# Performance work log

Measured on AMD Instinct MI355X. Metric: run time of the kernel, lower is better.

## Reference

```python
import jax, jax.numpy as jnp
import numpy as np

B, N, D, FF, L = 32, 1000, 128, 512, 6
EPS = 1e-5  # InstanceNorm1d default eps


def _inorm(x, g, b):
    # InstanceNorm1d on [B, d, N] == normalize over sequence dim N per channel (biased var)
    m = jnp.mean(x, axis=1, keepdims=True)
    v = jnp.var(x, axis=1, keepdims=True)
    return (x - m) / jnp.sqrt(v + EPS) * g + b


def setup_inputs() -> dict:
    key = jax.random.key(0)
    ks = jax.random.split(key, 10)
    s = 0.05
    data = jax.random.normal(ks[0], (B, N, 2), dtype=jnp.float32)
    # negative pairwise distances (module calls it negative_dist)
    dist = -jax.random.uniform(ks[1], (B, N, N), dtype=jnp.float32)
    log_scale = jnp.ones((1,), dtype=jnp.float32)
    We = jax.random.normal(ks[2], (D, 2), dtype=jnp.float32) * s
    be = jnp.zeros((D,), dtype=jnp.float32)
    Wq = jax.random.normal(ks[3], (L, D, D), dtype=jnp.float32) * s
    Wk = jax.random.normal(ks[4], (L, D, D), dtype=jnp.float32) * s
    Wv = jax.random.normal(ks[5], (L, D, D), dtype=jnp.float32) * s
    g1 = jnp.ones((L, D), dtype=jnp.float32)
    b1 = jnp.zeros((L, D), dtype=jnp.float32)
    W1 = jax.random.normal(ks[6], (L, FF, D), dtype=jnp.float32) * s
    bw1 = jnp.zeros((L, FF), dtype=jnp.float32)
    W2 = jax.random.normal(ks[7], (L, D, FF), dtype=jnp.float32) * s
    bw2 = jnp.zeros((L, D), dtype=jnp.float32)
    g2 = jnp.ones((L, D), dtype=jnp.float32)
    b2 = jnp.zeros((L, D), dtype=jnp.float32)
    alpha = jnp.ones((L,), dtype=jnp.float32)  # AFT_dist_alpha per layer
    return dict(data=data, dist=dist, log_scale=log_scale, We=We, be=be,
                Wq=Wq, Wk=Wk, Wv=Wv, g1=g1, b1=b1, W1=W1, bw1=bw1,
                W2=W2, bw2=bw2, g2=g2, b2=b2, alpha=alpha)


def reference(data, dist, log_scale, We, be, Wq, Wk, Wv, g1, b1, W1, bw1, W2, bw2, g2, b2, alpha):
    x = data @ We.T + be  # [B,N,D]
    for i in range(L):
        q = x @ Wq[i].T
        k = x @ Wk[i].T
        v = x @ Wv[i].T
        A = jnp.exp(log_scale[0] * alpha[i] * dist)  # [B,N,N]
        ek = jnp.exp(k)
        bias = jnp.einsum('bnm,bmd->bnd', A, ek * v)
        denom = jnp.einsum('bnm,bmd->bnd', A, ek)
        out = jax.nn.sigmoid(q) * (bias / denom)
        x1 = _inorm(x + out, g1[i], b1[i])
        h = jax.nn.relu(x1 @ W1[i].T + bw1[i]) @ W2[i].T + bw2[i]
        x = _inorm(x1 + h, g2[i], b2[i])
    return x
```

## Files before the change

kernel.cpp:

```cpp
#include <hip/hip_runtime.h>
#include <hip/hip_bf16.h>

typedef __attribute__((ext_vector_type(4))) float f32x4;
typedef __attribute__((ext_vector_type(8))) short bf16x8;
typedef __attribute__((ext_vector_type(4))) short s16x4;

#define LCOUNT 6

static __device__ __forceinline__ unsigned short f2b(float f){
  __hip_bfloat16 h = __float2bfloat16(f);
  return __builtin_bit_cast(unsigned short, h);
}
static __device__ __forceinline__ float b2f(unsigned short u){
  unsigned int x = ((unsigned int)u) << 16;
  return __builtin_bit_cast(float, x);
}
static __device__ __forceinline__ void gl16(const void* g, void* l){
  __builtin_amdgcn_global_load_lds(
      (const __attribute__((address_space(1))) void*)g,
      (__attribute__((address_space(3))) void*)l, 16, 0, 0);
}
static __device__ __forceinline__ f32x4 mfma16(bf16x8 a, bf16x8 b, f32x4 c){
  return __builtin_amdgcn_mfma_f32_16x16x32_bf16(a, b, c, 0, 0, 0);
}

__global__ void k_cvt5(const float* __restrict__ Wq, const float* __restrict__ Wk,
                       const float* __restrict__ Wv, const float* __restrict__ W1,
                       const float* __restrict__ W2,
                       unsigned short* __restrict__ wqb, unsigned short* __restrict__ wkb,
                       unsigned short* __restrict__ wvb, unsigned short* __restrict__ w1b,
                       unsigned short* __restrict__ w2b){
  int i = blockIdx.x*256 + threadIdx.x;
  if (i < 98304) wqb[i] = f2b(Wq[i]);
  else if (i < 196608) wkb[i-98304] = f2b(Wk[i-98304]);
  else if (i < 294912) wvb[i-196608] = f2b(Wv[i-196608]);
  else if (i < 688128) w1b[i-294912] = f2b(W1[i-294912]);
  else w2b[i-688128] = f2b(W2[i-688128]);
}

__global__ void k_cvtdist(const float* __restrict__ dist, unsigned short* __restrict__ db){
  int t = blockIdx.x*256 + threadIdx.x;
  int row = t >> 7, ch = t & 127;
  bf16x8 w;
  if (ch >= 125){
#pragma unroll
    for (int e=0;e<8;e++) w[e] = 0;
  } else {
    const float* p = dist + (size_t)row*1000 + ch*8;
    f32x4 a = *(const f32x4*)p;
    f32x4 b = *(const f32x4*)(p + 4);
#pragma unroll
    for (int e=0;e<4;e++){ w[e] = (short)f2b(a[e]); w[4+e] = (short)f2b(b[e]); }
  }
  *(bf16x8*)&db[(size_t)row*1024 + ch*8] = w;
}

__global__ void k_embed(const float* __restrict__ data, const float* __restrict__ We,
                        const float* __restrict__ be, float* __restrict__ x,
                        unsigned short* __restrict__ xb){
  int idx = blockIdx.x*256 + threadIdx.x;
  int d = idx & 127, bn = idx >> 7;
  float v = data[bn*2]*We[d*2] + data[bn*2+1]*We[d*2+1] + be[d];
  x[idx] = v; xb[idx] = f2b(v);
}

__global__ void k_scale(const float* __restrict__ part, int cnt,
                        const float* __restrict__ g, const float* __restrict__ beta,
                        float* __restrict__ na, float* __restrict__ nc){
  int b = blockIdx.x, d = threadIdx.x;
  float s1 = 0.f, s2 = 0.f;
  for (int c = 0; c < cnt; ++c){
    size_t pi = (((size_t)b*cnt + c)*128 + d)*2;
    s1 += part[pi]; s2 += part[pi+1];
  }
  float mean = s1 * 1e-3f;
  float var  = s2 * 1e-3f - mean*mean;
  float a = g[d] * rsqrtf(var + 1e-5f);
  na[b*128 + d] = a; nc[b*128 + d] = beta[d] - mean*a;
}

__global__ __launch_bounds__(256) void k_fapply(
  const float* __restrict__ x, const float* __restrict__ na,
  const float* __restrict__ nc, float* __restrict__ dout){
  int blk = blockIdx.x, tid = threadIdx.x;
  int b = blk / 125;
  size_t base = (size_t)blk*1024 + tid*4;
  int d0 = (tid*4) & 127;
  f32x4 v = *(const f32x4*)&x[base];
  f32x4 o;
#pragma unroll
  for (int e=0;e<4;e++) o[e] = v[e]*na[b*128 + d0 + e] + nc[b*128 + d0 + e];
  *(f32x4*)&dout[base] = o;
}

template<int NORM>
__global__ __launch_bounds__(256) void k_qkv(
  const unsigned short* __restrict__ xb, const float* __restrict__ x,
  const float* __restrict__ na2, const float* __restrict__ nc2,
  const unsigned short* __restrict__ Wqb, const unsigned short* __restrict__ Wkb,
  const unsigned short* __restrict__ Wvb,
  unsigned short* __restrict__ sigq, unsigned short* __restrict__ Zc)
{
  __shared__ unsigned short LA[2*2048];
  __shared__ unsigned short LB[2][4][256][8];
  __shared__ float sna[128], snc[128];
  int tid = threadIdx.x, wid = tid>>6, lane = tid&63;
  int l15 = lane&15, lg = lane>>4;
  int wm = wid>>1, wn = wid&1;
  int bt = blockIdx.x, b = bt>>4, t = bt&15;
  int kv = blockIdx.y;
  int lrow = t*64 + lane; if (lrow > 999) lrow = 999;
  size_t arow = (size_t)(b*1000 + lrow);

  if (NORM){
    if (tid < 128){ sna[tid] = na2[b*128 + tid]; snc[tid] = nc2[b*128 + tid]; }
    __syncthreads();
  }

  f32x4 zf = {0.f,0.f,0.f,0.f};
  f32x4 acc[2][4], acc2[2][4];
#pragma unroll
  for (int i=0;i<2;i++)
#pragma unroll
    for (int j=0;j<4;j++){ acc[i][j] = zf; acc2[i][j] = zf; }

  auto stage = [&](int kk, int buf){
    int k0 = kk*32;
    if (NORM){
      const float* p = x + arow*128 + k0 + wid*8;
      f32x4 v0 = *(const f32x4*)p;
      f32x4 v1 = *(const f32x4*)(p + 4);
      bf16x8 w;
#pragma unroll
      for (int e=0;e<4;e++){
        int k = k0 + wid*8;
        w[e]   = (short)f2b(v0[e]*sna[k+e]   + snc[k+e]);
        w[4+e] = (short)f2b(v1[e]*sna[k+4+e] + snc[k+4+e]);
      }
      *(bf16x8*)&LA[buf*2048 + wid*512 + lane*8] = w;
    } else {
      gl16(xb + arow*128 + k0 + wid*8, &LA[buf*2048 + wid*512]);
    }
    if (kv == 0){
#pragma unroll
      for (int t2=0;t2<2;++t2){
        int e = wid + t2*4, g2 = e>>1, nb = e&1;
        gl16(Wqb + (size_t)(nb*64+lane)*128 + k0 + g2*8, &LB[buf][g2][nb*64][0]);
      }
    } else {
#pragma unroll
      for (int t2=0;t2<4;++t2){
        int e = wid + t2*4, g2 = e&3, nb = e>>2;
        const unsigned short* src = (nb < 2)
          ? Wkb + (size_t)(nb*64+lane)*128 + k0 + g2*8
          : Wvb + (size_t)((nb-2)*64+lane)*128 + k0 + g2*8;
        gl16(src, &LB[buf][g2][nb*64][0]);
      }
    }
  };
  auto compute = [&](int buf){
    bf16x8 af[2];
#pragma unroll
    for (int i=0;i<2;i++){
      int row = wm*32 + i*16 + l15;
      af[i] = *(const bf16x8*)&LA[buf*2048 + lg*512 + row*8];
    }
#pragma unroll
    for (int j=0;j<4;j++){
      bf16x8 bq = *(const bf16x8*)&LB[buf][lg][wn*64 + j*16 + l15][0];
#pragma unroll
      for (int i=0;i<2;i++) acc[i][j] = mfma16(af[i], bq, acc[i][j]);
      if (kv){
        bf16x8 bv = *(const bf16x8*)&LB[buf][lg][128 + wn*64 + j*16 + l15][0];
#pragma unroll
        for (int i=0;i<2;i++) acc2[i][j] = mfma16(af[i], bv, acc2[i][j]);
      }
    }
  };

  stage(0, 0);
  __syncthreads();
  for (int kk = 0; kk < 4; ++kk){
    int buf = kk & 1;
    if (kk < 3) stage(kk+1, buf^1);
    compute(buf);
    __syncthreads();
  }

#pragma unroll
  for (int i=0;i<2;i++){
    int m4 = t*64 + wm*32 + i*16 + lg*4;
    if (m4 >= 1000) continue;
#pragma unroll
    for (int j=0;j<4;j++){
      int col = wn*64 + j*16 + l15;
      if (kv == 0){
#pragma unroll
        for (int r=0;r<4;r++)
          sigq[(size_t)(b*1000 + m4 + r)*128 + col] = f2b(1.f/(1.f + __expf(-acc[i][j][r])));
      } else {
        s16x4 pv, pk;
#pragma unroll
        for (int r=0;r<4;r++){
          float ek = __expf(acc[i][j][r]);
          pk[r] = (short)f2b(ek);
          pv[r] = (short)f2b(ek * acc2[i][j][r]);
        }
        size_t base = ((size_t)(b*128 + (m4>>3))*256 + col)*8 + ((m4>>2)&1)*4;
        *(s16x4*)&Zc[base] = pv;
        *(s16x4*)&Zc[base + 1024] = pk;
      }
    }
  }
}

template<int NORM, int USE16>
__global__ __launch_bounds__(256) void k_attn(
  const float* __restrict__ dist, const unsigned short* __restrict__ db16,
  const unsigned short* __restrict__ Zc, const unsigned short* __restrict__ sigq,
  float* __restrict__ x, float* __restrict__ partA,
  const float* __restrict__ na2, const float* __restrict__ nc2,
  const float* __restrict__ log_scale, const float* __restrict__ alpha, int layer)
{
  union SM {
    struct { unsigned short A[2][8][64][8]; unsigned short B[2][8][256][8]; } st;
    float den[64][128];
  };
  __shared__ SM sm;
  int tid = threadIdx.x, wid = tid>>6, lane = tid&63;
  int l15 = lane&15, lg = lane>>4;
  int bb = blockIdx.y, t = blockIdx.x, n0 = t*64;
  float sc = log_scale[0]*alpha[layer];
  const unsigned short* Zb = Zc + ((size_t)bb << 18);
  int an = n0 + lane; if (an > 999) an = 999;
  const size_t drow = (size_t)(bb*1000 + an);

  f32x4 zf = {0.f,0.f,0.f,0.f};
  f32x4 acc[4][4];
#pragma unroll
  for (int i=0;i<4;i++)
#pragma unroll
    for (int j=0;j<4;j++) acc[i][j] = zf;

  auto issueB = [&](int kk, int buf){
#pragma unroll
    for (int t2=0;t2<8;++t2){
      int e = wid + t2*4;
      int g2 = e >> 2, cb = e & 3;
      gl16(Zb + ((size_t)((kk*8 + g2)*256 + cb*64 + lane))*8, &sm.st.B[buf][g2][cb*64][0]);
    }
  };
  auto loadA2 = [&](int kk, float* v0, float* v1){
    int k0 = kk*64 + wid*8;
    int k1 = k0 + 32;
    if (USE16){
      bf16x8 r0 = *(const bf16x8*)(db16 + drow*1024 + k0);
      bf16x8 r1 = *(const bf16x8*)(db16 + drow*1024 + k1);
#pragma unroll
      for (int e=0;e<8;e++){ v0[e] = b2f((unsigned short)r0[e]); v1[e] = b2f((unsigned short)r1[e]); }
    } else {
      const float* dp = dist + drow*1000;
#pragma unroll
      for (int e=0;e<8;e++){
        int m0 = k0 + e; if (m0 > 999) m0 = 999;
        int m1 = k1 + e; if (m1 > 999) m1 = 999;
        v0[e] = dp[m0]; v1[e] = dp[m1];
      }
    }
  };
  auto expwrite2 = [&](const float* v0, const float* v1, int buf){
    bf16x8 w0, w1;
#pragma unroll
    for (int e=0;e<8;e++){
      w0[e] = (short)f2b(__expf(sc*v0[e]));
      w1[e] = (short)f2b(__expf(sc*v1[e]));
    }
    *(bf16x8*)&sm.st.A[buf][wid][lane][0]     = w0;
    *(bf16x8*)&sm.st.A[buf][wid+4][lane][0]   = w1;
  };
  auto compute = [&](int buf){
#pragma unroll
    for (int ks=0; ks<2; ++ks){
      bf16x8 af[4], bq[4];
#pragma unroll
      for (int i=0;i<4;i++) af[i] = *(const bf16x8*)&sm.st.A[buf][ks*4+lg][i*16 + l15][0];
#pragma unroll
      for (int j=0;j<4;j++) bq[j] = *(const bf16x8*)&sm.st.B[buf][ks*4+lg][wid*64 + j*16 + l15][0];
#pragma unroll
      for (int i=0;i<4;i++)
#pragma unroll
        for (int j=0;j<4;j++)
          acc[i][j] = mfma16(af[i], bq[j], acc[i][j]);
    }
  };

  float av0[8], av1[8];
  issueB(0, 0);
  loadA2(0, av0, av1);
  expwrite2(av0, av1, 0);
  __syncthreads();
  for (int kk = 0; kk < 16; ++kk){
    int buf = kk & 1;
    float nv0[8], nv1[8];
    if (kk < 15){ issueB(kk+1, buf^1); loadA2(kk+1, nv0, nv1); }
    compute(buf);
    if (kk < 15) expwrite2(nv0, nv1, buf^1);
    __syncthreads();
  }

  if (wid >= 2){
#pragma unroll
    for (int i=0;i<4;i++)
#pragma unroll
      for (int j=0;j<4;j++){
        int dcol = (wid-2)*64 + j*16 + l15;
#pragma unroll
        for (int r=0;r<4;r++)
          sm.den[i*16 + lg*4 + r][dcol] = acc[i][j][r];
      }
  }
  __syncthreads();
  if (wid < 2){
    float nav[4], ncv[4];
    if (NORM){
#pragma unroll
      for (int j=0;j<4;j++){
        int d = wid*64 + j*16 + l15;
        nav[j] = na2[bb*128 + d]; ncv[j] = nc2[bb*128 + d];
      }
    }
    float s1[4] = {0.f,0.f,0.f,0.f}, s2[4] = {0.f,0.f,0.f,0.f};
#pragma unroll
    for (int i=0;i<4;i++){
#pragma unroll
      for (int r=0;r<4;r++){
        int n = n0 + i*16 + lg*4 + r;
        if (n < 1000){
          size_t rowi = ((size_t)bb*1000 + n)*128;
#pragma unroll
          for (int j=0;j<4;j++){
            int d = wid*64 + j*16 + l15;
            float xv = x[rowi + d];
            if (NORM) xv = xv*nav[j] + ncv[j];
            float y = xv + b2f(sigq[rowi + d]) * acc[i][j][r] / sm.den[i*16 + lg*4 + r][d];
            x[rowi + d] = y;
            s1[j] += y; s2[j] += y*y;
          }
        }
      }
    }
#pragma unroll
    for (int j=0;j<4;j++){
      s1[j] += __shfl_xor(s1[j], 16); s2[j] += __shfl_xor(s2[j], 16);
      s1[j] += __shfl_xor(s1[j], 32); s2[j] += __shfl_xor(s2[j], 32);
    }
    if (lg == 0){
#pragma unroll
      for (int j=0;j<4;j++){
        int d = wid*64 + j*16 + l15;
        size_t pi = (((size_t)bb*16 + t)*128 + d)*2;
        partA[pi] = s1[j]; partA[pi+1] = s2[j];
      }
    }
  }
}

__global__ __launch_bounds__(512) void k_ff1(
  const float* __restrict__ x, const float* __restrict__ partA,
  const float* __restrict__ g1, const float* __restrict__ b1,
  const unsigned short* __restrict__ W1b, const float* __restrict__ bw1,
  float* __restrict__ x1, unsigned short* __restrict__ h1)
{
  __shared__ unsigned short LA[2][4][64][8];
  __shared__ unsigned short LB[2][4][512][8];
  __shared__ float sna[128], snc[128];
  int tid = threadIdx.x, wid = tid>>6, lane = tid&63;
  int l15 = lane&15, lg = lane>>4;
  int wm = wid>>2, wn = wid&3;
  int bt = blockIdx.x, b = bt>>4, t = bt&15;

  if (tid < 128){
    float s1 = 0.f, s2 = 0.f;
    for (int c = 0; c < 16; ++c){
      size_t pi = (((size_t)b*16 + c)*128 + tid)*2;
      s1 += partA[pi]; s2 += partA[pi+1];
    }
    float mean = s1 * 1e-3f;
    float var  = s2 * 1e-3f - mean*mean;
    float a = g1[tid] * rsqrtf(var + 1e-5f);
    sna[tid] = a; snc[tid] = b1[tid] - mean*a;
  }
  __syncthreads();

  f32x4 zf = {0.f,0.f,0.f,0.f};
  f32x4 acc[2][8];
#pragma unroll
  for (int i=0;i<2;i++)
#pragma unroll
    for (int j=0;j<8;j++) acc[i][j] = zf;

  auto stage = [&](int kk, int buf){
    int k0 = kk*32;
    if (tid < 256){
      int row = tid & 63, g2 = tid >> 6;
      int lr = t*64 + row;
      int rr = lr > 999 ? 999 : lr;
      const float* p = x + ((size_t)(b*1000 + rr))*128 + k0 + g2*8;
      f32x4 v0 = *(const f32x4*)p;
      f32x4 v1 = *(const f32x4*)(p + 4);
      f32x4 o0, o1;
      bf16x8 w;
#pragma unroll
      for (int e=0;e<4;e++){
        int k = k0 + g2*8;
        o0[e] = v0[e]*sna[k+e]   + snc[k+e];
        o1[e] = v1[e]*sna[k+4+e] + snc[k+4+e];
        w[e]   = (short)f2b(o0[e]);
        w[4+e] = (short)f2b(o1[e]);
      }
      *(bf16x8*)&LA[buf][g2][row][0] = w;
      if (lr < 1000){
        float* q = x1 + ((size_t)(b*1000 + lr))*128 + k0 + g2*8;
        *(f32x4*)q = o0; *(f32x4*)(q+4) = o1;
      }
    }
#pragma unroll
    for (int t2=0;t2<4;++t2){
      int e = wid*4 + t2;
      int g2 = e & 3, nb = e >> 2;
      gl16(W1b + (size_t)(nb*64 + lane)*128 + k0 + g2*8, &LB[buf][g2][nb*64][0]);
    }
  };
  auto compute = [&](int buf){
    bf16x8 af[2];
#pragma unroll
    for (int i=0;i<2;i++) af[i] = *(const bf16x8*)&LA[buf][lg][wm*32 + i*16 + l15][0];
#pragma unroll
    for (int j=0;j<8;j++){
      bf16x8 bq = *(const bf16x8*)&LB[buf][lg][wn*128 + j*16 + l15][0];
#pragma unroll
      for (int i=0;i<2;i++) acc[i][j] = mfma16(af[i], bq, acc[i][j]);
    }
  };

  stage(0, 0);
  __syncthreads();
  for (int kk = 0; kk < 4; ++kk){
    int buf = kk & 1;
    if (kk < 3) stage(kk+1, buf^1);
    compute(buf);
    __syncthreads();
  }

#pragma unroll
  for (int i=0;i<2;i++){
    int m4 = t*64 + wm*32 + i*16 + lg*4;
    if (m4 >= 1000) continue;
#pragma unroll
    for (int j=0;j<8;j++){
      int col = wn*128 + j*16 + l15;
      float bz = bw1[col];
#pragma unroll
      for (int r=0;r<4;r++){
        float v = acc[i][j][r] + bz;
        h1[(size_t)(b*1000 + m4 + r)*512 + col] = f2b(v > 0.f ? v : 0.f);
      }
    }
  }
}

__global__ __launch_bounds__(256) void k_ff2(
  const unsigned short* __restrict__ h1, const unsigned short* __restrict__ W2b,
  const float* __restrict__ bw2, const float* __restrict__ x1,
  float* __restrict__ x, float* __restrict__ partF)
{
  __shared__ unsigned short LA[2][4][64][8];
  __shared__ unsigned short LB[2][4][128][8];
  int tid = threadIdx.x, wid = tid>>6, lane = tid&63;
  int l15 = lane&15, lg = lane>>4;
  int wm = wid>>1, wn = wid&1;
  int bt = blockIdx.x, b = bt>>4, t = bt&15;
  int lrow = t*64 + lane; if (lrow > 999) lrow = 999;
  size_t arow = (size_t)(b*1000 + lrow);

  f32x4 zf = {0.f,0.f,0.f,0.f};
  f32x4 acc[2][4];
#pragma unroll
  for (int i=0;i<2;i++)
#pragma unroll
    for (int j=0;j<4;j++) acc[i][j] = zf;

  auto stage = [&](int kk, int buf){
    int k0 = kk*32;
    gl16(h1 + arow*512 + k0 + wid*8, &LA[buf][wid][0][0]);
#pragma unroll
    for (int t2=0;t2<2;++t2){
      int e = wid + t2*4, g2 = e>>1, nb = e&1;
      gl16(W2b + (size_t)(nb*64 + lane)*512 + k0 + g2*8, &LB[buf][g2][nb*64][0]);
    }
  };
  auto compute = [&](int buf){
    bf16x8 af[2];
#pragma unroll
    for (int i=0;i<2;i++) af[i] = *(const bf16x8*)&LA[buf][lg][wm*32 + i*16 + l15][0];
#pragma unroll
    for (int j=0;j<4;j++){
      bf16x8 bq = *(const bf16x8*)&LB[buf][lg][wn*64 + j*16 + l15][0];
#pragma unroll
      for (int i=0;i<2;i++) acc[i][j] = mfma16(af[i], bq, acc[i][j]);
    }
  };

  stage(0, 0);
  __syncthreads();
  for (int kk = 0; kk < 16; ++kk){
    int buf = kk & 1;
    if (kk < 15) stage(kk+1, buf^1);
    compute(buf);
    __syncthreads();
  }

  float s1[4] = {0.f,0.f,0.f,0.f}, s2[4] = {0.f,0.f,0.f,0.f};
#pragma unroll
  for (int i=0;i<2;i++){
    int m4 = t*64 + wm*32 + i*16 + lg*4;
    if (m4 >= 1000) continue;
#pragma unroll
    for (int j=0;j<4;j++){
      int col = wn*64 + j*16 + l15;
      float bz = bw2[col];
#pragma unroll
      for (int r=0;r<4;r++){
        size_t idx = (size_t)(b*1000 + m4 + r)*128 + col;
        float y = acc[i][j][r] + bz + x1[idx];
        x[idx] = y;
        s1[j] += y; s2[j] += y*y;
      }
    }
  }
#pragma unroll
  for (int j=0;j<4;j++){
    s1[j] += __shfl_xor(s1[j], 16); s2[j] += __shfl_xor(s2[j], 16);
    s1[j] += __shfl_xor(s1[j], 32); s2[j] += __shfl_xor(s2[j], 32);
  }
  if (lg == 0){
#pragma unroll
    for (int j=0;j<4;j++){
      int d = wn*64 + j*16 + l15;
      size_t pi = (((size_t)b*32 + t*2 + wm)*128 + d)*2;
      partF[pi] = s1[j]; partF[pi+1] = s2[j];
    }
  }
}

extern "C" void kernel_launch(void* const* d_in, const int* in_sizes, int n_in,
                              void* d_out, int out_size, void* d_ws, size_t ws_size,
                              hipStream_t stream) {
  const float* data = (const float*)d_in[0];
  const float* dist = (const float*)d_in[1];
  const float* log_scale = (const float*)d_in[2];
  const float* We = (const float*)d_in[3];
  const float* be = (const float*)d_in[4];
  const float* Wq = (const float*)d_in[5];
  const float* Wk = (const float*)d_in[6];
  const float* Wv = (const float*)d_in[7];
  const float* g1 = (const float*)d_in[8];
  const float* b1 = (const float*)d_in[9];
  const float* W1 = (const float*)d_in[10];
  const float* bw1 = (const float*)d_in[11];
  const float* W2 = (const float*)d_in[12];
  const float* bw2 = (const float*)d_in[13];
  const float* g2 = (const float*)d_in[14];
  const float* b2 = (const float*)d_in[15];
  const float* alpha = (const float*)d_in[16];
  float* dout = (float*)d_out;

  char* ws = (char*)d_ws;
  size_t off = 0;
  auto alloc = [&](size_t bytes) -> void* {
    void* p = ws + off; off += (bytes + 255) & ~(size_t)255; return p;
  };
  unsigned short* xb  = (unsigned short*)alloc(8192000);
  float* x            = (float*)alloc(16384000);
  unsigned short* sigq= (unsigned short*)alloc(8192000);
  unsigned short* Zc  = (unsigned short*)alloc(16777216);
  unsigned short* h1  = (unsigned short*)alloc(32768000);
  float* x1           = (float*)alloc(16384000);
  float* partA        = (float*)alloc(524288);
  float* partF        = (float*)alloc(1048576);
  float* na2          = (float*)alloc(16384);
  float* nc2          = (float*)alloc(16384);
  unsigned short* wqb = (unsigned short*)alloc(196608);
  unsigned short* wkb = (unsigned short*)alloc(196608);
  unsigned short* wvb = (unsigned short*)alloc(196608);
  unsigned short* w1b = (unsigned short*)alloc(786432);
  unsigned short* w2b = (unsigned short*)alloc(786432);
  if (off > ws_size) return;
  unsigned short* db16p = nullptr;
  if (ws_size >= off + 131072256) db16p = (unsigned short*)alloc(131072000);

  hipMemsetAsync(Zc, 0, 16777216, stream);
  k_cvt5<<<4224, 256, 0, stream>>>(Wq, Wk, Wv, W1, W2, wqb, wkb, wvb, w1b, w2b);
  if (db16p) k_cvtdist<<<16000, 256, 0, stream>>>(dist, db16p);
  k_embed<<<16000, 256, 0, stream>>>(data, We, be, x, xb);

  for (int i = 0; i < LCOUNT; ++i){
    if (i > 0)
      k_scale<<<32, 128, 0, stream>>>(partF, 32, g2 + (i-1)*128, b2 + (i-1)*128, na2, nc2);
    if (i == 0)
      k_qkv<0><<<dim3(512,2), 256, 0, stream>>>(xb, x, nullptr, nullptr,
                                                wqb + i*16384, wkb + i*16384, wvb + i*16384,
                                                sigq, Zc);
    else
      k_qkv<1><<<dim3(512,2), 256, 0, stream>>>(nullptr, x, na2, nc2,
                                                wqb + i*16384, wkb + i*16384, wvb + i*16384,
                                                sigq, Zc);
    if (i == 0){
      if (db16p) k_attn<0,1><<<dim3(16,32), 256, 0, stream>>>(dist, db16p, Zc, sigq, x, partA,
                                                              nullptr, nullptr, log_scale, alpha, i);
      else       k_attn<0,0><<<dim3(16,32), 256, 0, stream>>>(dist, nullptr, Zc, sigq, x, partA,
                                                              nullptr, nullptr, log_scale, alpha, i);
    } else {
      if (db16p) k_attn<1,1><<<dim3(16,32), 256, 0, stream>>>(dist, db16p, Zc, sigq, x, partA,
                                                              na2, nc2, log_scale, alpha, i);
      else       k_attn<1,0><<<dim3(16,32), 256, 0, stream>>>(dist, nullptr, Zc, sigq, x, partA,
                                                              na2, nc2, log_scale, alpha, i);
    }
    k_ff1<<<512, 512, 0, stream>>>(x, partA, g1 + i*128, b1 + i*128,
                                   w1b + i*65536, bw1 + i*512, x1, h1);
    k_ff2<<<512, 256, 0, stream>>>(h1, w2b + i*65536, bw2 + i*128, x1, x, partF);
  }
  k_scale<<<32, 128, 0, stream>>>(partF, 32, g2 + 5*128, b2 + 5*128, na2, nc2);
  k_fapply<<<4000, 256, 0, stream>>>(x, na2, nc2, dout);
}
```

Before: 831.4 us.

## Load attention B operand directly into registers instead of staging through LDS

The Zc (exp(k)*v / exp(k)) operand tiles are now fetched from global memory straight into per-wave register fragments, double-buffered in registers, rather than copied into LDS with global_load_lds and read back. The main loop is unrolled by two to alternate register sets, and LDS holds only the exp(dist) A tiles. This removes LDS traffic and shrinks shared memory, which may raise occupancy. The cost is extra VGPR pressure, and the non-16-bit path now rounds dist to bf16 before the exponent.

Measured after the change: 896.5 us. +7.8%, slower.

```diff
diff --git a/kernel.cpp b/kernel.cpp
--- a/kernel.cpp
+++ b/kernel.cpp
@@ -223,7 +223,7 @@
   const float* __restrict__ log_scale, const float* __restrict__ alpha, int layer)
 {
   union SM {
-    struct { unsigned short A[2][8][64][8]; unsigned short B[2][8][256][8]; } st;
+    unsigned short A[2][8][64][8];
     float den[64][128];
   };
   __shared__ SM sm;
@@ -242,69 +242,67 @@
 #pragma unroll
     for (int j=0;j<4;j++) acc[i][j] = zf;
 
-  auto issueB = [&](int kk, int buf){
-#pragma unroll
-    for (int t2=0;t2<8;++t2){
-      int e = wid + t2*4;
-      int g2 = e >> 2, cb = e & 3;
-      gl16(Zb + ((size_t)((kk*8 + g2)*256 + cb*64 + lane))*8, &sm.st.B[buf][g2][cb*64][0]);
-    }
-  };
-  auto loadA2 = [&](int kk, float* v0, float* v1){
-    int k0 = kk*64 + wid*8;
-    int k1 = k0 + 32;
+  auto loadBset = [&](int kk, bf16x8 (&r)[8]){
+#pragma unroll
+    for (int ks=0; ks<2; ++ks)
+#pragma unroll
+      for (int j=0; j<4; ++j)
+        r[ks*4+j] = *(const bf16x8*)(Zb +
+            ((size_t)((kk*8 + ks*4 + lg)*256 + wid*64 + j*16 + l15))*8);
+  };
+  auto loadAraw = [&](int kk, bf16x8& r0, bf16x8& r1){
+    int k0 = kk*64 + wid*8, k1 = k0 + 32;
     if (USE16){
-      bf16x8 r0 = *(const bf16x8*)(db16 + drow*1024 + k0);
-      bf16x8 r1 = *(const bf16x8*)(db16 + drow*1024 + k1);
-#pragma unroll
-      for (int e=0;e<8;e++){ v0[e] = b2f((unsigned short)r0[e]); v1[e] = b2f((unsigned short)r1[e]); }
+      r0 = *(const bf16x8*)(db16 + drow*1024 + k0);
+      r1 = *(const bf16x8*)(db16 + drow*1024 + k1);
     } else {
       const float* dp = dist + drow*1000;
 #pragma unroll
       for (int e=0;e<8;e++){
-        int m0 = k0 + e; if (m0 > 999) m0 = 999;
-        int m1 = k1 + e; if (m1 > 999) m1 = 999;
-        v0[e] = dp[m0]; v1[e] = dp[m1];
-      }
-    }
-  };
-  auto expwrite2 = [&](const float* v0, const float* v1, int buf){
+        int m0 = k0+e; if (m0>999) m0=999;
+        int m1 = k1+e; if (m1>999) m1=999;
+        r0[e] = (short)f2b(dp[m0]); r1[e] = (short)f2b(dp[m1]);
+      }
+    }
+  };
+  auto expwrite2 = [&](bf16x8 r0, bf16x8 r1, int buf){
     bf16x8 w0, w1;
 #pragma unroll
     for (int e=0;e<8;e++){
-      w0[e] = (short)f2b(__expf(sc*v0[e]));
-      w1[e] = (short)f2b(__expf(sc*v1[e]));
-    }
-    *(bf16x8*)&sm.st.A[buf][wid][lane][0]     = w0;
-    *(bf16x8*)&sm.st.A[buf][wid+4][lane][0]   = w1;
-  };
-  auto compute = [&](int buf){
+      w0[e] = (short)f2b(__expf(sc*b2f((unsigned short)r0[e])));
+      w1[e] = (short)f2b(__expf(sc*b2f((unsigned short)r1[e])));
+    }
+    *(bf16x8*)&sm.A[buf][wid][lane][0]   = w0;
+    *(bf16x8*)&sm.A[buf][wid+4][lane][0] = w1;
+  };
+  auto computeR = [&](const bf16x8 (&r)[8], int abuf){
 #pragma unroll
     for (int ks=0; ks<2; ++ks){
-      bf16x8 af[4], bq[4];
-#pragma unroll
-      for (int i=0;i<4;i++) af[i] = *(const bf16x8*)&sm.st.A[buf][ks*4+lg][i*16 + l15][0];
-#pragma unroll
-      for (int j=0;j<4;j++) bq[j] = *(const bf16x8*)&sm.st.B[buf][ks*4+lg][wid*64 + j*16 + l15][0];
+      bf16x8 af[4];
+#pragma unroll
+      for (int i=0;i<4;i++) af[i] = *(const bf16x8*)&sm.A[abuf][ks*4+lg][i*16 + l15][0];
 #pragma unroll
       for (int i=0;i<4;i++)
 #pragma unroll
         for (int j=0;j<4;j++)
-          acc[i][j] = mfma16(af[i], bq[j], acc[i][j]);
-    }
-  };
-
-  float av0[8], av1[8];
-  issueB(0, 0);
-  loadA2(0, av0, av1);
-  expwrite2(av0, av1, 0);
+          acc[i][j] = mfma16(af[i], r[ks*4+j], acc[i][j]);
+    }
+  };
+
+  bf16x8 rA[8], rB[8], a0, a1;
+  loadAraw(0, a0, a1);
+  loadBset(0, rA);
+  expwrite2(a0, a1, 0);
   __syncthreads();
-  for (int kk = 0; kk < 16; ++kk){
-    int buf = kk & 1;
-    float nv0[8], nv1[8];
-    if (kk < 15){ issueB(kk+1, buf^1); loadA2(kk+1, nv0, nv1); }
-    compute(buf);
-    if (kk < 15) expwrite2(nv0, nv1, buf^1);
+  for (int kk = 0; kk < 16; kk += 2){
+    loadAraw(kk+1, a0, a1);
+    loadBset(kk+1, rB);
+    computeR(rA, 0);
+    expwrite2(a0, a1, 1);
+    __syncthreads();
+    if (kk+2 < 16){ loadAraw(kk+2, a0, a1); loadBset(kk+2, rA); }
+    computeR(rB, 1);
+    if (kk+2 < 16) expwrite2(a0, a1, 0);
     __syncthreads();
   }
 
```
